# Optimization experiments

Measured on AMD Instinct MI355X. Metric: run time of the kernel, lower is better.

## Reference

```python
import jax, jax.numpy as jnp
import numpy as np

B, H, KVH, D, CACHE = 16, 32, 8, 128, 4096


def _rope(x, cos, sin):
    # x: [B, S, Hx, D]; cos/sin: [B, S, 1, D//2] -- complex rotation on (even, odd) pairs
    xe, xo = x[..., ::2], x[..., 1::2]
    re = xe * cos - xo * sin
    im = xe * sin + xo * cos
    return jnp.stack([re, im], axis=-1).reshape(x.shape)


def setup_inputs() -> dict:
    key = jax.random.key(0)
    ks = jax.random.split(key, 8)
    xq = jax.random.normal(ks[0], (B, 1, H, D), jnp.float32)
    xk = jax.random.normal(ks[1], (B, 1, KVH, D), jnp.float32)
    xv = jax.random.normal(ks[2], (B, 1, KVH, D), jnp.float32)
    input_pos = jax.random.randint(ks[3], (B,), 1024, CACHE - 1, dtype=jnp.int32)
    inv_freq = 1.0 / (10000.0 ** (jnp.arange(0, D, 2, dtype=jnp.float32) / D))
    ang = input_pos.astype(jnp.float32)[:, None] * inv_freq[None, :]  # [B, D/2]
    freqs_cos = jnp.cos(ang)[:, None, :]  # [B, 1, D/2]
    freqs_sin = jnp.sin(ang)[:, None, :]
    cache_k = jax.random.randint(ks[4], (B, KVH, CACHE, D), -127, 128, dtype=jnp.int32)
    cache_v = jax.random.randint(ks[5], (B, KVH, CACHE, D), -127, 128, dtype=jnp.int32)
    k_scaler = jax.random.uniform(ks[6], (B, KVH, CACHE), jnp.float32, minval=0.005, maxval=0.05)
    v_scaler = jax.random.uniform(ks[7], (B, KVH, CACHE), jnp.float32, minval=0.005, maxval=0.05)
    return dict(xq=xq, xk=xk, xv=xv, freqs_cos=freqs_cos, freqs_sin=freqs_sin,
                k_scaler=k_scaler, v_scaler=v_scaler, cache_k=cache_k, cache_v=cache_v,
                input_pos=input_pos)


def reference(xq, xk, xv, freqs_cos, freqs_sin, k_scaler, v_scaler, cache_k, cache_v, input_pos):
    B_, S_, H_, D_ = xq.shape
    KVH_ = xk.shape[2]
    n_rep = H_ // KVH_
    cos, sin = freqs_cos[:, :, None, :], freqs_sin[:, :, None, :]
    q = _rope(xq, cos, sin)
    k = _rope(xk, cos, sin)
    # new decode token, [B, KVH, D]
    k_new = jnp.transpose(k, (0, 2, 1, 3))[:, :, 0, :]
    v_new = jnp.transpose(xv, (0, 2, 1, 3))[:, :, 0, :]
    # per-token, per-kv-head int8 quantization of the new K/V
    k_s = jnp.max(jnp.abs(k_new), axis=-1, keepdims=True) / 127.0 + 1e-8
    v_s = jnp.max(jnp.abs(v_new), axis=-1, keepdims=True) / 127.0 + 1e-8
    k_q = jnp.clip(jnp.round(k_new / k_s), -127, 127).astype(cache_k.dtype)
    v_q = jnp.clip(jnp.round(v_new / v_s), -127, 127).astype(cache_v.dtype)
    b_idx = jnp.arange(B_)
    cache_k = cache_k.at[b_idx, :, input_pos].set(k_q)
    cache_v = cache_v.at[b_idx, :, input_pos].set(v_q)
    k_scaler = k_scaler.at[b_idx, :, input_pos].set(k_s[..., 0])
    v_scaler = v_scaler.at[b_idx, :, input_pos].set(v_s[..., 0])
    # GQA: group query heads per kv head instead of materializing repeat_kv
    qg = jnp.transpose(q, (0, 2, 1, 3)).reshape(B_, KVH_, n_rep, D_)  # S_ == 1
    scores = jnp.einsum('bkrd,bksd->bkrs', qg, cache_k.astype(jnp.float32))
    scores = scores / jnp.sqrt(jnp.float32(D_)) * k_scaler[:, :, None, :]  # inline K dequant
    S_cache = cache_k.shape[2]
    mask = jnp.where(jnp.arange(S_cache)[None, :] <= input_pos[:, None], 0.0, -1e30)
    probs = jax.nn.softmax(scores + mask[:, None, None, :].astype(scores.dtype), axis=-1)
    out = jnp.einsum('bkrs,bksd->bkrd', probs * v_scaler[:, :, None, :], cache_v.astype(jnp.float32))
    return out.reshape(B_, H_, 1, D_)
```

## Files before the change

### kernel.cpp

```cpp
#include <hip/hip_runtime.h>
#include <hip/hip_bf16.h>
#include <cstdint>
#include <cstddef>

#define BATCH 16
#define HQ 32
#define KVHN 8
#define NREP 4
#define DIM 128
#define CACHE_LEN 4096
#define STATE_POS 128
#define NSTATE (CACHE_LEN / STATE_POS)

__device__ __forceinline__ float half_reduce_sum(float v) {
    #pragma unroll
    for (int mask = 16; mask; mask >>= 1) v += __shfl_xor(v, mask, 64);
    return v;
}

__global__ void attn_partial(
    const float* __restrict__ xq,
    const float* __restrict__ fcos,
    const float* __restrict__ fsin,
    const float* __restrict__ k_scaler,
    const float* __restrict__ v_scaler,
    const int*   __restrict__ cache_k,
    const int*   __restrict__ cache_v,
    const int*   __restrict__ input_pos,
    float* __restrict__ ws_acc,
    float* __restrict__ ws_ml)
{
    const int state = blockIdx.x;
    const int kvh   = blockIdx.y;
    const int b     = blockIdx.z;
    const int pos   = input_pos[b];
    const int start = state * STATE_POS;
    if (start >= pos) return;

    const int lane = threadIdx.x;
    const int half = lane >> 5;
    const int hl   = lane & 31;
    const int d0   = hl * 4;

    float q[4][4];
    {
        const float2 c2 = *(const float2*)(fcos + b * 64 + 2 * hl);
        const float2 s2 = *(const float2*)(fsin + b * 64 + 2 * hl);
        #pragma unroll
        for (int r = 0; r < 4; ++r) {
            const float4 x = *(const float4*)(xq + ((size_t)(b * HQ + kvh * NREP + r)) * DIM + d0);
            q[r][0] = x.x * c2.x - x.y * s2.x;
            q[r][1] = x.x * s2.x + x.y * c2.x;
            q[r][2] = x.z * c2.y - x.w * s2.y;
            q[r][3] = x.z * s2.y + x.w * c2.y;
        }
    }

    const int bk = b * KVHN + kvh;
    const int*   __restrict__ kb = cache_k + (size_t)bk * CACHE_LEN * DIM;
    const int*   __restrict__ vb = cache_v + (size_t)bk * CACHE_LEN * DIM;
    const float* __restrict__ ks = k_scaler + (size_t)bk * CACHE_LEN;
    const float* __restrict__ vs = v_scaler + (size_t)bk * CACHE_LEN;

    float m[4] = {-1e30f, -1e30f, -1e30f, -1e30f};
    float l[4] = {0.f, 0.f, 0.f, 0.f};
    float acc[4][4] = {};

    const int send = min(start + STATE_POS, pos);
    const float rsD = 0.088388347648318447f;

    for (int i = 0; ; ++i) {
        const int slo = start + 2 * i;
        if (slo >= send) break;
        const int s = slo + half;
        const bool valid = s < send;

        const int4 kk = *(const int4*)(kb + (size_t)s * DIM + d0);
        const float k0 = (float)kk.x, k1 = (float)kk.y, k2 = (float)kk.z, k3 = (float)kk.w;
        float p[4];
        #pragma unroll
        for (int r = 0; r < 4; ++r)
            p[r] = q[r][0] * k0 + q[r][1] * k1 + q[r][2] * k2 + q[r][3] * k3;
        #pragma unroll
        for (int mask = 16; mask; mask >>= 1) {
            #pragma unroll
            for (int r = 0; r < 4; ++r) p[r] += __shfl_xor(p[r], mask, 64);
        }

        const float scale = ks[s] * rsD;
        const int4 vv = *(const int4*)(vb + (size_t)s * DIM + d0);
        const float v0 = (float)vv.x, v1 = (float)vv.y, v2 = (float)vv.z, v3 = (float)vv.w;
        const float vsc = vs[s];

        #pragma unroll
        for (int r = 0; r < 4; ++r) {
            float sc = p[r] * scale;
            if (!valid) sc = -1e30f;
            const float mn = fmaxf(m[r], sc);
            const float alpha = __expf(m[r] - mn);
            float pr = __expf(sc - mn);
            if (!valid) pr = 0.f;
            m[r] = mn;
            l[r] = l[r] * alpha + pr;
            const float pv = pr * vsc;
            acc[r][0] = acc[r][0] * alpha + pv * v0;
            acc[r][1] = acc[r][1] * alpha + pv * v1;
            acc[r][2] = acc[r][2] * alpha + pv * v2;
            acc[r][3] = acc[r][3] * alpha + pv * v3;
        }
    }

    float4 A[4]; float Mv[4], Lv[4];
    #pragma unroll
    for (int r = 0; r < 4; ++r) {
        const float mo = __shfl_xor(m[r], 32, 64);
        const float lo = __shfl_xor(l[r], 32, 64);
        float ao0 = __shfl_xor(acc[r][0], 32, 64);
        float ao1 = __shfl_xor(acc[r][1], 32, 64);
        float ao2 = __shfl_xor(acc[r][2], 32, 64);
        float ao3 = __shfl_xor(acc[r][3], 32, 64);
        const float M  = fmaxf(m[r], mo);
        const float a1 = __expf(m[r] - M);
        const float a2 = __expf(mo   - M);
        Mv[r] = M;
        Lv[r] = l[r] * a1 + lo * a2;
        A[r].x = acc[r][0] * a1 + ao0 * a2;
        A[r].y = acc[r][1] * a1 + ao1 * a2;
        A[r].z = acc[r][2] * a1 + ao2 * a2;
        A[r].w = acc[r][3] * a1 + ao3 * a2;
    }

    if (half == 0) {
        float* abase = ws_acc + (((size_t)bk * NSTATE + state) * 4) * DIM;
        #pragma unroll
        for (int r = 0; r < 4; ++r)
            *(float4*)(abase + r * DIM + d0) = A[r];
        if (lane == 0) {
            float* mlb = ws_ml + ((size_t)bk * NSTATE + state) * 8;
            #pragma unroll
            for (int r = 0; r < 4; ++r) { mlb[2 * r] = Mv[r]; mlb[2 * r + 1] = Lv[r]; }
        }
    }
}

__global__ __launch_bounds__(256) void attn_combine(
    const float* __restrict__ xq,
    const float* __restrict__ xk,
    const float* __restrict__ xv,
    const float* __restrict__ fcos,
    const float* __restrict__ fsin,
    const int*   __restrict__ input_pos,
    const float* __restrict__ ws_acc,
    const float* __restrict__ ws_ml,
    float* __restrict__ out)
{
    const int bk  = blockIdx.x;
    const int b   = bk >> 3;
    const int kvh = bk & 7;
    const int pos = input_pos[b];
    const int nst = min(NSTATE, (pos + STATE_POS - 1) / STATE_POS);

    const int t    = threadIdx.x;
    const int lane = t & 63;
    const int w    = t >> 6;

    __shared__ float sq[4][DIM];
    __shared__ float skq[DIM];
    __shared__ float svd[DIM];
    __shared__ float sml[NSTATE][8];
    __shared__ float ssc[4];
    __shared__ float sks, svs;

    const float rsD = 0.088388347648318447f;

    {
        const float c  = fcos[b * 64 + lane];
        const float s  = fsin[b * 64 + lane];
        const size_t qb = ((size_t)(b * HQ + kvh * NREP + w)) * DIM;
        const float xe = xq[qb + 2 * lane];
        const float xo = xq[qb + 2 * lane + 1];
        sq[w][2 * lane]     = xe * c - xo * s;
        sq[w][2 * lane + 1] = xe * s + xo * c;
    }
    if (w == 0) {
        const float c  = fcos[b * 64 + lane];
        const float s  = fsin[b * 64 + lane];
        const size_t kbb = ((size_t)(b * KVHN + kvh)) * DIM;
        const float xe = xk[kbb + 2 * lane];
        const float xo = xk[kbb + 2 * lane + 1];
        skq[2 * lane]     = xe * c - xo * s;
        skq[2 * lane + 1] = xe * s + xo * c;
    }
    if (t < nst * 8) sml[t >> 3][t & 7] = ws_ml[(size_t)bk * NSTATE * 8 + t];
    __syncthreads();

    if (w == 0) {
        float a = fmaxf(fabsf(skq[lane]), fabsf(skq[64 + lane]));
        #pragma unroll
        for (int mask = 32; mask; mask >>= 1) a = fmaxf(a, __shfl_xor(a, mask, 64));
        if (lane == 0) sks = a / 127.0f + 1e-8f;
    } else if (w == 1) {
        const size_t vbb = ((size_t)(b * KVHN + kvh)) * DIM;
        float a = fmaxf(fabsf(xv[vbb + lane]), fabsf(xv[vbb + 64 + lane]));
        #pragma unroll
        for (int mask = 32; mask; mask >>= 1) a = fmaxf(a, __shfl_xor(a, mask, 64));
        if (lane == 0) svs = a / 127.0f + 1e-8f;
    }
    __syncthreads();

    if (t < DIM) {
        skq[t] = fminf(fmaxf(rintf(skq[t] / sks), -127.f), 127.f);
    } else {
        const int d = t - DIM;
        const size_t vbb = ((size_t)(b * KVHN + kvh)) * DIM;
        const float vq = fminf(fmaxf(rintf(xv[vbb + d] / svs), -127.f), 127.f);
        svd[d] = vq * svs;
    }
    __syncthreads();

    {
        float sum = sq[w][lane] * skq[lane] + sq[w][64 + lane] * skq[64 + lane];
        #pragma unroll
        for (int mask = 32; mask; mask >>= 1) sum += __shfl_xor(sum, mask, 64);
        if (lane == 0) ssc[w] = sum * rsD * sks;
    }
    __syncthreads();

    const int r  = w;
    const int db = lane;
    float M = ssc[r];
    for (int s2 = 0; s2 < nst; ++s2) M = fmaxf(M, sml[s2][2 * r]);
    const float pn = __expf(ssc[r] - M);
    float L  = pn;
    float o0 = pn * svd[db];
    float o1 = pn * svd[db + 64];
    const float* ab = ws_acc + (size_t)bk * NSTATE * 4 * DIM;
    for (int s2 = 0; s2 < nst; ++s2) {
        const float al = __expf(sml[s2][2 * r] - M);
        L  += sml[s2][2 * r + 1] * al;
        o0 += ab[((size_t)(s2 * 4 + r)) * DIM + db]      * al;
        o1 += ab[((size_t)(s2 * 4 + r)) * DIM + db + 64] * al;
    }
    const float invL = 1.0f / L;
    float* ob = out + ((size_t)(b * HQ + kvh * NREP + r)) * DIM;
    ob[db]      = o0 * invL;
    ob[db + 64] = o1 * invL;
}

extern "C" void kernel_launch(void* const* d_in, const int* in_sizes, int n_in,
                              void* d_out, int out_size, void* d_ws, size_t ws_size,
                              hipStream_t stream)
{
    const float* xq        = (const float*)d_in[0];
    const float* xk        = (const float*)d_in[1];
    const float* xv        = (const float*)d_in[2];
    const float* fcos      = (const float*)d_in[3];
    const float* fsin      = (const float*)d_in[4];
    const float* k_scaler  = (const float*)d_in[5];
    const float* v_scaler  = (const float*)d_in[6];
    const int*   cache_k   = (const int*)d_in[7];
    const int*   cache_v   = (const int*)d_in[8];
    const int*   input_pos = (const int*)d_in[9];
    float* out = (float*)d_out;

    float* ws_acc = (float*)d_ws;
    float* ws_ml  = ws_acc + (size_t)BATCH * KVHN * NSTATE * 4 * DIM;

    dim3 g1(NSTATE, KVHN, BATCH);
    attn_partial<<<g1, 64, 0, stream>>>(xq, fcos, fsin, k_scaler, v_scaler,
                                        cache_k, cache_v, input_pos, ws_acc, ws_ml);
    attn_combine<<<BATCH * KVHN, 256, 0, stream>>>(xq, xk, xv, fcos, fsin,
                                                   input_pos, ws_acc, ws_ml, out);
}
```

Measured before the change: 538.7 us.

## Restructure partial attention into two-pass score/max then PV accumulation

Replaces the online-softmax loop, which processed two positions per wave with 32 lanes each, with a two-pass scheme. Each of four lane groups handles one position at a time, with 8 dims per lane. The first pass computes scores into shared memory and tracks the max, and the second pass does exp and V accumulation without per-step rescaling. Fewer shuffle steps per position and no alpha rescales are intended to cut ALU and latency work. The cost is LDS traffic, a barrier, more registers for acc[4][8], and loads of always-full 128-position tiles that may read beyond the valid length up to the tile edge.

Result: faster. 503.7 us (-6.5%).

```diff
diff --git a/kernel.cpp b/kernel.cpp
--- a/kernel.cpp
+++ b/kernel.cpp
@@ -12,13 +12,7 @@
 #define STATE_POS 128
 #define NSTATE (CACHE_LEN / STATE_POS)
 
-__device__ __forceinline__ float half_reduce_sum(float v) {
-    #pragma unroll
-    for (int mask = 16; mask; mask >>= 1) v += __shfl_xor(v, mask, 64);
-    return v;
-}
-
-__global__ void attn_partial(
+__global__ __launch_bounds__(64) void attn_partial(
     const float* __restrict__ xq,
     const float* __restrict__ fcos,
     const float* __restrict__ fsin,
@@ -38,21 +32,32 @@
     if (start >= pos) return;
 
     const int lane = threadIdx.x;
-    const int half = lane >> 5;
-    const int hl   = lane & 31;
-    const int d0   = hl * 4;
-
-    float q[4][4];
+    const int g    = lane >> 4;
+    const int sl   = lane & 15;
+    const int d0   = sl * 8;
+
+    const int send = min(start + STATE_POS, pos);
+    const float rsD = 0.088388347648318447f;
+
+    float q[4][8];
     {
-        const float2 c2 = *(const float2*)(fcos + b * 64 + 2 * hl);
-        const float2 s2 = *(const float2*)(fsin + b * 64 + 2 * hl);
-        #pragma unroll
-        for (int r = 0; r < 4; ++r) {
-            const float4 x = *(const float4*)(xq + ((size_t)(b * HQ + kvh * NREP + r)) * DIM + d0);
-            q[r][0] = x.x * c2.x - x.y * s2.x;
-            q[r][1] = x.x * s2.x + x.y * c2.x;
-            q[r][2] = x.z * c2.y - x.w * s2.y;
-            q[r][3] = x.z * s2.y + x.w * c2.y;
+        float4 c4 = *(const float4*)(fcos + b * 64 + sl * 4);
+        float4 s4 = *(const float4*)(fsin + b * 64 + sl * 4);
+        c4.x *= rsD; c4.y *= rsD; c4.z *= rsD; c4.w *= rsD;
+        s4.x *= rsD; s4.y *= rsD; s4.z *= rsD; s4.w *= rsD;
+        #pragma unroll
+        for (int r = 0; r < 4; ++r) {
+            const float* qp = xq + ((size_t)(b * HQ + kvh * NREP + r)) * DIM + d0;
+            const float4 x0 = *(const float4*)qp;
+            const float4 x1 = *(const float4*)(qp + 4);
+            q[r][0] = x0.x * c4.x - x0.y * s4.x;
+            q[r][1] = x0.x * s4.x + x0.y * c4.x;
+            q[r][2] = x0.z * c4.y - x0.w * s4.y;
+            q[r][3] = x0.z * s4.y + x0.w * c4.y;
+            q[r][4] = x1.x * c4.z - x1.y * s4.z;
+            q[r][5] = x1.x * s4.z + x1.y * c4.z;
+            q[r][6] = x1.z * c4.w - x1.w * s4.w;
+            q[r][7] = x1.z * s4.w + x1.w * c4.w;
         }
     }
 
@@ -62,83 +67,98 @@
     const float* __restrict__ ks = k_scaler + (size_t)bk * CACHE_LEN;
     const float* __restrict__ vs = v_scaler + (size_t)bk * CACHE_LEN;
 
-    float m[4] = {-1e30f, -1e30f, -1e30f, -1e30f};
-    float l[4] = {0.f, 0.f, 0.f, 0.f};
-    float acc[4][4] = {};
-
-    const int send = min(start + STATE_POS, pos);
-    const float rsD = 0.088388347648318447f;
-
-    for (int i = 0; ; ++i) {
-        const int slo = start + 2 * i;
-        if (slo >= send) break;
-        const int s = slo + half;
-        const bool valid = s < send;
-
-        const int4 kk = *(const int4*)(kb + (size_t)s * DIM + d0);
-        const float k0 = (float)kk.x, k1 = (float)kk.y, k2 = (float)kk.z, k3 = (float)kk.w;
+    __shared__ float4 ssc4[STATE_POS];
+
+    float mloc[4] = {-1e30f, -1e30f, -1e30f, -1e30f};
+
+    #pragma unroll 4
+    for (int i = 0; i < STATE_POS / 4; ++i) {
+        const int s = start + i * 4 + g;
+        const int* kp = kb + (size_t)s * DIM + d0;
+        const int4 kk0 = *(const int4*)kp;
+        const int4 kk1 = *(const int4*)(kp + 4);
+        const float k0 = (float)kk0.x, k1 = (float)kk0.y, k2 = (float)kk0.z, k3 = (float)kk0.w;
+        const float k4 = (float)kk1.x, k5 = (float)kk1.y, k6 = (float)kk1.z, k7 = (float)kk1.w;
         float p[4];
         #pragma unroll
-        for (int r = 0; r < 4; ++r)
-            p[r] = q[r][0] * k0 + q[r][1] * k1 + q[r][2] * k2 + q[r][3] * k3;
-        #pragma unroll
-        for (int mask = 16; mask; mask >>= 1) {
+        for (int r = 0; r < 4; ++r) {
+            p[r] = q[r][0] * k0 + q[r][1] * k1 + q[r][2] * k2 + q[r][3] * k3
+                 + q[r][4] * k4 + q[r][5] * k5 + q[r][6] * k6 + q[r][7] * k7;
+        }
+        #pragma unroll
+        for (int mask = 1; mask <= 8; mask <<= 1) {
             #pragma unroll
             for (int r = 0; r < 4; ++r) p[r] += __shfl_xor(p[r], mask, 64);
         }
-
-        const float scale = ks[s] * rsD;
-        const int4 vv = *(const int4*)(vb + (size_t)s * DIM + d0);
-        const float v0 = (float)vv.x, v1 = (float)vv.y, v2 = (float)vv.z, v3 = (float)vv.w;
-        const float vsc = vs[s];
-
-        #pragma unroll
-        for (int r = 0; r < 4; ++r) {
-            float sc = p[r] * scale;
-            if (!valid) sc = -1e30f;
-            const float mn = fmaxf(m[r], sc);
-            const float alpha = __expf(m[r] - mn);
-            float pr = __expf(sc - mn);
-            if (!valid) pr = 0.f;
-            m[r] = mn;
-            l[r] = l[r] * alpha + pr;
-            const float pv = pr * vsc;
-            acc[r][0] = acc[r][0] * alpha + pv * v0;
-            acc[r][1] = acc[r][1] * alpha + pv * v1;
-            acc[r][2] = acc[r][2] * alpha + pv * v2;
-            acc[r][3] = acc[r][3] * alpha + pv * v3;
-        }
-    }
-
-    float4 A[4]; float Mv[4], Lv[4];
+        const float scale = ks[s];
+        const bool valid = s < send;
+        float4 sc;
+        sc.x = valid ? p[0] * scale : -1e30f;
+        sc.y = valid ? p[1] * scale : -1e30f;
+        sc.z = valid ? p[2] * scale : -1e30f;
+        sc.w = valid ? p[3] * scale : -1e30f;
+        mloc[0] = fmaxf(mloc[0], sc.x);
+        mloc[1] = fmaxf(mloc[1], sc.y);
+        mloc[2] = fmaxf(mloc[2], sc.z);
+        mloc[3] = fmaxf(mloc[3], sc.w);
+        if (sl == 0) ssc4[i * 4 + g] = sc;
+    }
+
     #pragma unroll
     for (int r = 0; r < 4; ++r) {
-        const float mo = __shfl_xor(m[r], 32, 64);
-        const float lo = __shfl_xor(l[r], 32, 64);
-        float ao0 = __shfl_xor(acc[r][0], 32, 64);
-        float ao1 = __shfl_xor(acc[r][1], 32, 64);
-        float ao2 = __shfl_xor(acc[r][2], 32, 64);
-        float ao3 = __shfl_xor(acc[r][3], 32, 64);
-        const float M  = fmaxf(m[r], mo);
-        const float a1 = __expf(m[r] - M);
-        const float a2 = __expf(mo   - M);
-        Mv[r] = M;
-        Lv[r] = l[r] * a1 + lo * a2;
-        A[r].x = acc[r][0] * a1 + ao0 * a2;
-        A[r].y = acc[r][1] * a1 + ao1 * a2;
-        A[r].z = acc[r][2] * a1 + ao2 * a2;
-        A[r].w = acc[r][3] * a1 + ao3 * a2;
-    }
-
-    if (half == 0) {
+        mloc[r] = fmaxf(mloc[r], __shfl_xor(mloc[r], 16, 64));
+        mloc[r] = fmaxf(mloc[r], __shfl_xor(mloc[r], 32, 64));
+    }
+    __syncthreads();
+
+    float l[4] = {0.f, 0.f, 0.f, 0.f};
+    float acc[4][8] = {};
+    #pragma unroll 4
+    for (int i = 0; i < STATE_POS / 4; ++i) {
+        const int s = start + i * 4 + g;
+        const int* vp = vb + (size_t)s * DIM + d0;
+        const int4 vv0 = *(const int4*)vp;
+        const int4 vv1 = *(const int4*)(vp + 4);
+        const float vsc = vs[s];
+        const float4 sc = ssc4[i * 4 + g];
+        const float v0 = (float)vv0.x, v1 = (float)vv0.y, v2 = (float)vv0.z, v3 = (float)vv0.w;
+        const float v4 = (float)vv1.x, v5 = (float)vv1.y, v6 = (float)vv1.z, v7 = (float)vv1.w;
+        const float scr[4] = {sc.x, sc.y, sc.z, sc.w};
+        #pragma unroll
+        for (int r = 0; r < 4; ++r) {
+            const float pr = __expf(scr[r] - mloc[r]);
+            l[r] += pr;
+            const float pv = pr * vsc;
+            acc[r][0] += pv * v0; acc[r][1] += pv * v1;
+            acc[r][2] += pv * v2; acc[r][3] += pv * v3;
+            acc[r][4] += pv * v4; acc[r][5] += pv * v5;
+            acc[r][6] += pv * v6; acc[r][7] += pv * v7;
+        }
+    }
+
+    #pragma unroll
+    for (int mask = 16; mask <= 32; mask <<= 1) {
+        #pragma unroll
+        for (int r = 0; r < 4; ++r) {
+            l[r] += __shfl_xor(l[r], mask, 64);
+            #pragma unroll
+            for (int c = 0; c < 8; ++c) acc[r][c] += __shfl_xor(acc[r][c], mask, 64);
+        }
+    }
+
+    if (g == 0) {
         float* abase = ws_acc + (((size_t)bk * NSTATE + state) * 4) * DIM;
         #pragma unroll
-        for (int r = 0; r < 4; ++r)
-            *(float4*)(abase + r * DIM + d0) = A[r];
-        if (lane == 0) {
+        for (int r = 0; r < 4; ++r) {
+            float4 a0 = make_float4(acc[r][0], acc[r][1], acc[r][2], acc[r][3]);
+            float4 a1 = make_float4(acc[r][4], acc[r][5], acc[r][6], acc[r][7]);
+            *(float4*)(abase + r * DIM + d0)     = a0;
+            *(float4*)(abase + r * DIM + d0 + 4) = a1;
+        }
+        if (sl == 0) {
             float* mlb = ws_ml + ((size_t)bk * NSTATE + state) * 8;
             #pragma unroll
-            for (int r = 0; r < 4; ++r) { mlb[2 * r] = Mv[r]; mlb[2 * r + 1] = Lv[r]; }
+            for (int r = 0; r < 4; ++r) { mlb[2 * r] = mloc[r]; mlb[2 * r + 1] = l[r]; }
         }
     }
 }
```
